# Kernel tuning notes

Measured on AMD Instinct MI355X. Metric: run time of the kernel, lower is better.

The kernel has to match this reference:

```python
import jax, jax.numpy as jnp
import numpy as np

N_EMBED = 256
B, T = 2, 8192


def setup_inputs() -> dict:
    key = jax.random.key(0)
    ks = jax.random.split(key, 7)
    s = 1.0 / np.sqrt(N_EMBED)  # ~nn.Linear init scale
    return {
        "x": jax.random.normal(ks[0], (B, T, N_EMBED), dtype=jnp.float32),
        "Wq": jax.random.normal(ks[1], (N_EMBED, N_EMBED), dtype=jnp.float32) * s,
        "bq": jax.random.normal(ks[2], (N_EMBED,), dtype=jnp.float32) * s,
        "Wk": jax.random.normal(ks[3], (N_EMBED, N_EMBED), dtype=jnp.float32) * s,
        "bk": jax.random.normal(ks[4], (N_EMBED,), dtype=jnp.float32) * s,
        "Wv": jax.random.normal(ks[5], (N_EMBED, N_EMBED), dtype=jnp.float32) * s,
        "bv": jax.random.normal(ks[6], (N_EMBED,), dtype=jnp.float32) * s,
    }


def reference(x, Wq, bq, Wk, bk, Wv, bv):
    # q/k/v projections: [B, T, D]
    q = x @ Wq + bq
    k = x @ Wk + bk
    v = x @ Wv + bv
    # Naive attention: full [B, T, T] score matrix, no scale, no mask.
    scores = jnp.einsum("btd,bsd->bts", q, k)
    attn = jax.nn.softmax(scores, axis=-1)
    return jnp.einsum("bts,bsd->btd", attn, v)
```

## Files before the change

### kernel.cpp

```cpp
#include <hip/hip_runtime.h>
#include <stdint.h>

typedef __attribute__((ext_vector_type(4))) float f32x4;
typedef __attribute__((ext_vector_type(16))) float f32x16;
typedef __attribute__((ext_vector_type(8))) short s16x8;
typedef __attribute__((ext_vector_type(4))) short s16x4;
typedef __attribute__((ext_vector_type(4))) unsigned int u32x4;
typedef __attribute__((ext_vector_type(8))) _Float16 f16x8;
typedef __attribute__((ext_vector_type(4))) _Float16 f16x4;

#define MFMA16(a, b, c) __builtin_amdgcn_mfma_f32_16x16x32_bf16((a), (b), (c), 0, 0, 0)
#define MFMA32H(a, b, c) __builtin_amdgcn_mfma_f32_32x32x16_f16((a), (b), (c), 0, 0, 0)


__device__ __forceinline__ unsigned short f2bf(float f) {
  unsigned int u = __float_as_uint(f);
  u += 0x7FFFu + ((u >> 16) & 1u);
  return (unsigned short)(u >> 16);
}
__device__ __forceinline__ float bf2f(unsigned short h) {
  return __uint_as_float(((unsigned int)h) << 16);
}

__global__ void wtrans_kernel(const float* __restrict__ Wq,
                              const float* __restrict__ Wk,
                              const float* __restrict__ Wv,
                              short* __restrict__ wt) {
  int idx = blockIdx.x * 256 + threadIdx.x;
  int w = idx >> 16;
  int rc = idx & 65535;
  int d = rc >> 8;
  int n = rc & 255;
  const float* Ws = (w == 0) ? Wq : ((w == 1) ? Wk : Wv);
  float v = Ws[rc];
  unsigned short hi = f2bf(v);
  unsigned short lo = f2bf(v - bf2f(hi));
  short* th = wt + w * 131072;
  th[n * 256 + d] = (short)hi;
  th[65536 + n * 256 + d] = (short)lo;
}

__global__ __launch_bounds__(256, 2)
void qkv_kernel(const float* __restrict__ x,
                const float* __restrict__ bq,
                const float* __restrict__ bk,
                const float* __restrict__ bv,
                const short* __restrict__ wt,
                short* __restrict__ Qf, short* __restrict__ Kf,
                short* __restrict__ Vt) {
  __shared__ short X[16896];
  int tid = threadIdx.x;
  int r0 = blockIdx.x * 32;
  int bidx = r0 >> 13;
  int tl0 = r0 & 8191;
#pragma unroll
  for (int i = 0; i < 8; i++) {
    int E = i * 1024 + tid * 4;
    int r = E >> 8, col = E & 255;
    f32x4 v = *(const f32x4*)(x + (size_t)(r0 + r) * 256 + col);
    s16x4 h, lo;
#pragma unroll
    for (int j = 0; j < 4; j++) {
      unsigned short hh = f2bf(v[j]);
      h[j] = (short)hh;
      lo[j] = (short)f2bf(v[j] - bf2f(hh));
    }
    *(s16x4*)&X[r * 264 + col] = h;
    *(s16x4*)&X[8448 + r * 264 + col] = lo;
  }
  __syncthreads();

  int lane = tid & 63, wv = tid >> 6;
  int quad = lane >> 4, lq = lane & 15;

  {
    int strip = wv & 1;
    const short* WhT = wt + ((wv < 2) ? 0 : 131072);
    const short* WlT = WhT + 65536;
    f32x4 acc[16];
#pragma unroll
    for (int nt = 0; nt < 16; nt++) acc[nt] = (f32x4){0.f, 0.f, 0.f, 0.f};
    int arow = (strip * 16 + lq) * 264 + quad * 8;
#pragma unroll
    for (int c = 0; c < 8; c++) {
      s16x8 xh = *(const s16x8*)&X[arow + c * 32];
      s16x8 xl = *(const s16x8*)&X[8448 + arow + c * 32];
#pragma unroll
      for (int nt = 0; nt < 16; nt++) {
        int boff = (nt * 16 + lq) * 256 + c * 32 + quad * 8;
        s16x8 wh = *(const s16x8*)(WhT + boff);
        s16x8 wl = *(const s16x8*)(WlT + boff);
        acc[nt] = MFMA16(xh, wh, acc[nt]);
        acc[nt] = MFMA16(xl, wh, acc[nt]);
        acc[nt] = MFMA16(xh, wl, acc[nt]);
      }
    }
    const float* bias = (wv < 2) ? bq : bk;
    _Float16* Of = (_Float16*)((wv < 2) ? Qf : Kf);
#pragma unroll
    for (int nt = 0; nt < 16; nt++) {
      int col = nt * 16 + lq;
      float bb = bias[col];
#pragma unroll
      for (int r = 0; r < 4; r++) {
        int row = r0 + strip * 16 + quad * 4 + r;
        Of[row * 256 + col] = (_Float16)(acc[nt][r] + bb);
      }
    }
  }
  {
    const short* WhT = wt + 262144;
    const short* WlT = wt + 327680;
    f32x4 acc[4][2];
#pragma unroll
    for (int mt = 0; mt < 4; mt++)
#pragma unroll
      for (int nt = 0; nt < 2; nt++) acc[mt][nt] = (f32x4){0.f, 0.f, 0.f, 0.f};
#pragma unroll
    for (int c = 0; c < 8; c++) {
      int co = c * 32 + quad * 8;
      s16x8 xh0 = *(const s16x8*)&X[lq * 264 + co];
      s16x8 xl0 = *(const s16x8*)&X[8448 + lq * 264 + co];
      s16x8 xh1 = *(const s16x8*)&X[(16 + lq) * 264 + co];
      s16x8 xl1 = *(const s16x8*)&X[8448 + (16 + lq) * 264 + co];
#pragma unroll
      for (int mt = 0; mt < 4; mt++) {
        int aoff = (wv * 64 + mt * 16 + lq) * 256 + co;
        s16x8 wh = *(const s16x8*)(WhT + aoff);
        s16x8 wl = *(const s16x8*)(WlT + aoff);
        acc[mt][0] = MFMA16(wh, xh0, acc[mt][0]);
        acc[mt][0] = MFMA16(wl, xh0, acc[mt][0]);
        acc[mt][0] = MFMA16(wh, xl0, acc[mt][0]);
        acc[mt][1] = MFMA16(wh, xh1, acc[mt][1]);
        acc[mt][1] = MFMA16(wl, xh1, acc[mt][1]);
        acc[mt][1] = MFMA16(wh, xl1, acc[mt][1]);
      }
    }
#pragma unroll
    for (int mt = 0; mt < 4; mt++) {
#pragma unroll
      for (int r = 0; r < 4; r++) {
        int drow = wv * 64 + mt * 16 + quad * 4 + r;
        float bb = bv[drow];
#pragma unroll
        for (int nt = 0; nt < 2; nt++) {
          ((_Float16*)Vt)[(bidx * 256 + drow) * 8192 + tl0 + nt * 16 + lq] =
              (_Float16)(acc[mt][nt][r] + bb);
        }
      }
    }
  }
}

__global__ __launch_bounds__(512, 2)
void attn_kernel(const short* __restrict__ Qf, const short* __restrict__ Kf,
                 const short* __restrict__ Vt,
                 float* __restrict__ out, float* __restrict__ O1,
                 float* __restrict__ Mlg) {
  __shared__ short sm[45568];
  short* KL  = sm;
  short* VtL = sm + 16896;
  short* PLb = sm + 35328;
  int tid = threadIdx.x;
  int lane = tid & 63, wv = tid >> 6;
  int lq32 = lane & 31, hh = lane >> 5, h8 = hh * 8;
  int strip = wv & 3, sh = wv >> 2;
  short* PL = PLb + wv * 1280;
  int blk = blockIdx.x;
  int qt = blk >> 1, sblk = blk & 1;
  int row0g = qt * 128;
  int b = row0g >> 13;
  int sbase = b * 8192 + sblk * 4096;

  f16x8 qf[16];
  {
    const _Float16* qrow =
        (const _Float16*)Qf + (size_t)(row0g + strip * 32 + lq32) * 256 + h8;
#pragma unroll
    for (int st = 0; st < 16; st++) qf[st] = *(const f16x8*)(qrow + st * 16);
  }
  float m_ = -__builtin_inff();
  float l_ = 0.f;
  f32x16 Oacc[8];
#pragma unroll
  for (int dt = 0; dt < 8; dt++)
#pragma unroll
    for (int i = 0; i < 16; i++) Oacc[dt][i] = 0.f;

  u32x4 k_r[4], vt_r[4];
#pragma unroll
  for (int i = 0; i < 4; i++) {
    int L = i * 512 + tid;
    int s = L >> 5, g = L & 31;
    int d = L >> 3, g2 = L & 7;
    k_r[i] = *(const u32x4*)(Kf + (size_t)(sbase + s) * 256 + g * 8);
    vt_r[i] = *(const u32x4*)(Vt + (size_t)(b * 256 + d) * 8192 +
                              sblk * 4096 + g2 * 8);
  }

  for (int it = 0; it < 64; it++) {
#pragma unroll
    for (int i = 0; i < 4; i++) {
      int L = i * 512 + tid;
      int s = L >> 5, g = L & 31;
      int d = L >> 3, g2 = L & 7;
      *(u32x4*)&KL[s * 264 + g * 8] = k_r[i];
      *(u32x4*)&VtL[d * 72 + g2 * 8] = vt_r[i];
    }
    __syncthreads();
    {
      int s0n = ((it + 1) & 63) * 64;
#pragma unroll
      for (int i = 0; i < 4; i++) {
        int L = i * 512 + tid;
        int s = L >> 5, g = L & 31;
        int d = L >> 3, g2 = L & 7;
        k_r[i] = *(const u32x4*)(Kf + (size_t)(sbase + s0n + s) * 256 + g * 8);
        vt_r[i] = *(const u32x4*)(Vt + (size_t)(b * 256 + d) * 8192 +
                                  sblk * 4096 + s0n + g2 * 8);
      }
    }
    f32x16 sacc;
#pragma unroll
    for (int i = 0; i < 16; i++) sacc[i] = 0.f;
    int krow = (sh * 32 + lq32) * 264 + h8;
#pragma unroll
    for (int st = 0; st < 16; st++) {
      f16x8 kf = *(const f16x8*)&KL[krow + st * 16];
      sacc = MFMA32H(kf, qf[st], sacc);
    }
    float mx = sacc[0];
#pragma unroll
    for (int i = 1; i < 16; i++) mx = fmaxf(mx, sacc[i]);
    mx = fmaxf(mx, __shfl_xor(mx, 32));
    float mn = fmaxf(m_, mx);
    float alpha = __expf(m_ - mn);
    m_ = mn;
    float rs = 0.f;
#pragma unroll
    for (int i = 0; i < 16; i++) {
      sacc[i] = __expf(sacc[i] - mn);
      rs += sacc[i];
    }
    rs += __shfl_xor(rs, 32);
    l_ = l_ * alpha + rs;
#pragma unroll
    for (int g = 0; g < 4; g++) {
      f16x4 pk;
#pragma unroll
      for (int j = 0; j < 4; j++) pk[j] = (_Float16)sacc[g * 4 + j];
      *(f16x4*)&PL[lq32 * 40 + 8 * g + 4 * hh] = pk;
    }
    if (!__all(alpha == 1.f)) {
#pragma unroll
      for (int dt = 0; dt < 8; dt++) Oacc[dt] = Oacc[dt] * alpha;
    }
    f16x8 pf0 = *(const f16x8*)&PL[lq32 * 40 + h8];
    f16x8 pf1 = *(const f16x8*)&PL[lq32 * 40 + 16 + h8];
#pragma unroll
    for (int dt = 0; dt < 8; dt++) {
      int vrow = (dt * 32 + lq32) * 72 + sh * 32;
      f16x8 vf0 = *(const f16x8*)&VtL[vrow + h8];
      f16x8 vf1 = *(const f16x8*)&VtL[vrow + 16 + h8];
      Oacc[dt] = MFMA32H(vf0, pf0, Oacc[dt]);
      Oacc[dt] = MFMA32H(vf1, pf1, Oacc[dt]);
    }
    __syncthreads();
  }

  float* smf = (float*)sm;
  float* Msh = smf + 16896;
  if (lane < 32) {
    Msh[(sh * 4 + strip) * 32 + lq32] = m_;
    Msh[256 + (sh * 4 + strip) * 32 + lq32] = l_;
  }
  __syncthreads();
  float m1 = Msh[((1 - sh) * 4 + strip) * 32 + lq32];
  float l1 = Msh[256 + ((1 - sh) * 4 + strip) * 32 + lq32];
  float mm = fmaxf(m_, m1);
  float e0 = __expf(m_ - mm);
  float e1 = __expf(m1 - mm);
  float* Opart = (sblk == 0) ? out : O1;
  if (sh == 0 && lane < 32) {
    float lsum = l_ * e0 + l1 * e1;
    int rowq = row0g + strip * 32 + lq32;
    Mlg[sblk * 32768 + rowq * 2] = mm;
    Mlg[sblk * 32768 + rowq * 2 + 1] = lsum;
  }
  float* Ob = smf + strip * 4224;
#pragma unroll
  for (int hd = 0; hd < 2; hd++) {
    __syncthreads();
    if (sh == 1) {
#pragma unroll
      for (int dt2 = 0; dt2 < 4; dt2++) {
        int dt = hd * 4 + dt2;
#pragma unroll
        for (int g = 0; g < 4; g++) {
          f32x4 v = {Oacc[dt][g * 4], Oacc[dt][g * 4 + 1],
                     Oacc[dt][g * 4 + 2], Oacc[dt][g * 4 + 3]};
          *(f32x4*)&Ob[lq32 * 132 + dt2 * 32 + 8 * g + 4 * hh] = v;
        }
      }
    }
    __syncthreads();
    if (sh == 0) {
#pragma unroll
      for (int dt2 = 0; dt2 < 4; dt2++) {
        int dt = hd * 4 + dt2;
#pragma unroll
        for (int g = 0; g < 4; g++) {
          float* ad = &Ob[lq32 * 132 + dt2 * 32 + 8 * g + 4 * hh];
          f32x4 o1 = *(f32x4*)ad;
          f32x4 cmb;
#pragma unroll
          for (int j = 0; j < 4; j++)
            cmb[j] = Oacc[dt][g * 4 + j] * e0 + o1[j] * e1;
          *(f32x4*)ad = cmb;
        }
      }
    }
    __syncthreads();
#pragma unroll
    for (int i = 0; i < 8; i++) {
      int idx = i * 512 + tid;
      int q = idx >> 5, gb = idx & 31;
      f32x4 v = *(f32x4*)&smf[(q >> 5) * 4224 + (q & 31) * 132 + gb * 4];
      *(f32x4*)&Opart[(size_t)(row0g + q) * 256 + hd * 128 + gb * 4] = v;
    }
  }
}

__global__ void merge_kernel(const float* __restrict__ O1,
                             const float* __restrict__ Mlg,
                             float* __restrict__ out) {
  int idx = blockIdx.x * 256 + threadIdx.x;
  int q = idx >> 6, dg = idx & 63;
  float m0 = Mlg[q * 2], l0 = Mlg[q * 2 + 1];
  float m1 = Mlg[32768 + q * 2], l1 = Mlg[32768 + q * 2 + 1];
  float mm = fmaxf(m0, m1);
  float e0 = __expf(m0 - mm), e1 = __expf(m1 - mm);
  float inv = 1.f / (l0 * e0 + l1 * e1);
  f32x4 a = *(const f32x4*)(out + (size_t)q * 256 + dg * 4);
  f32x4 bb = *(const f32x4*)(O1 + (size_t)q * 256 + dg * 4);
  f32x4 r;
#pragma unroll
  for (int j = 0; j < 4; j++) r[j] = (a[j] * e0 + bb[j] * e1) * inv;
  *(f32x4*)(out + (size_t)q * 256 + dg * 4) = r;
}

extern "C" void kernel_launch(void* const* d_in, const int* in_sizes, int n_in,
                              void* d_out, int out_size, void* d_ws, size_t ws_size,
                              hipStream_t stream) {
  const float* x  = (const float*)d_in[0];
  const float* Wq = (const float*)d_in[1];
  const float* bq = (const float*)d_in[2];
  const float* Wk = (const float*)d_in[3];
  const float* bk = (const float*)d_in[4];
  const float* Wv = (const float*)d_in[5];
  const float* bv = (const float*)d_in[6];
  float* out = (float*)d_out;
  short* ws = (short*)d_ws;
  short* wt = ws;
  short* Qf = ws + 393216;
  short* Kf = Qf + 4194304;
  short* Vt = Kf + 4194304;
  float* O1  = (float*)(ws + 12976128);
  float* Mlg = (float*)ws;
  hipLaunchKernelGGL(wtrans_kernel, dim3(768), dim3(256), 0, stream, Wq, Wk, Wv, wt);
  hipLaunchKernelGGL(qkv_kernel, dim3(512), dim3(256), 0, stream,
                     x, bq, bk, bv, wt, Qf, Kf, Vt);
  hipLaunchKernelGGL(attn_kernel, dim3(256), dim3(512), 0, stream,
                     Qf, Kf, Vt, out, O1, Mlg);
  hipLaunchKernelGGL(merge_kernel, dim3(4096), dim3(256), 0, stream,
                     O1, Mlg, out);
}
```

Before: 385.8 us.

## Double-buffer K/V tiles in LDS and pass P via lane shuffles

K and V tiles are now double-buffered in shared memory, so the next tile is written after compute and only one barrier per iteration is needed. The softmax probabilities are packed to fp16 and exchanged across half-waves with shuffles instead of going through a per-wave LDS scratch area. This cuts barrier stalls and LDS traffic, but enlarges shared memory, which likely reduces resident blocks per CU.

After: 410.4 us. +6.4%, slower.

```diff
diff --git a/kernel.cpp b/kernel.cpp
--- a/kernel.cpp
+++ b/kernel.cpp
@@ -7,7 +7,7 @@
 typedef __attribute__((ext_vector_type(4))) short s16x4;
 typedef __attribute__((ext_vector_type(4))) unsigned int u32x4;
 typedef __attribute__((ext_vector_type(8))) _Float16 f16x8;
-typedef __attribute__((ext_vector_type(4))) _Float16 f16x4;
+typedef __attribute__((ext_vector_type(2))) _Float16 f16x2;
 
 #define MFMA16(a, b, c) __builtin_amdgcn_mfma_f32_16x16x32_bf16((a), (b), (c), 0, 0, 0)
 #define MFMA32H(a, b, c) __builtin_amdgcn_mfma_f32_32x32x16_f16((a), (b), (c), 0, 0, 0)
@@ -20,6 +20,12 @@
 }
 __device__ __forceinline__ float bf2f(unsigned short h) {
   return __uint_as_float(((unsigned int)h) << 16);
+}
+__device__ __forceinline__ unsigned int packh2(float a, float b) {
+  f16x2 t;
+  t[0] = (_Float16)a;
+  t[1] = (_Float16)b;
+  return *(unsigned int*)&t;
 }
 
 __global__ void wtrans_kernel(const float* __restrict__ Wq,
@@ -157,15 +163,11 @@
                  const short* __restrict__ Vt,
                  float* __restrict__ out, float* __restrict__ O1,
                  float* __restrict__ Mlg) {
-  __shared__ short sm[45568];
-  short* KL  = sm;
-  short* VtL = sm + 16896;
-  short* PLb = sm + 35328;
+  __shared__ short sm[70656];
   int tid = threadIdx.x;
   int lane = tid & 63, wv = tid >> 6;
   int lq32 = lane & 31, hh = lane >> 5, h8 = hh * 8;
   int strip = wv & 3, sh = wv >> 2;
-  short* PL = PLb + wv * 1280;
   int blk = blockIdx.x;
   int qt = blk >> 1, sblk = blk & 1;
   int row0g = qt * 128;
@@ -197,19 +199,20 @@
     vt_r[i] = *(const u32x4*)(Vt + (size_t)(b * 256 + d) * 8192 +
                               sblk * 4096 + g2 * 8);
   }
+#pragma unroll
+  for (int i = 0; i < 4; i++) {
+    int L = i * 512 + tid;
+    int s = L >> 5, g = L & 31;
+    int d = L >> 3, g2 = L & 7;
+    *(u32x4*)&sm[s * 264 + g * 8] = k_r[i];
+    *(u32x4*)&sm[16896 + d * 72 + g2 * 8] = vt_r[i];
+  }
 
   for (int it = 0; it < 64; it++) {
-#pragma unroll
-    for (int i = 0; i < 4; i++) {
-      int L = i * 512 + tid;
-      int s = L >> 5, g = L & 31;
-      int d = L >> 3, g2 = L & 7;
-      *(u32x4*)&KL[s * 264 + g * 8] = k_r[i];
-      *(u32x4*)&VtL[d * 72 + g2 * 8] = vt_r[i];
-    }
+    short* cur = sm + (it & 1) * 35328;
     __syncthreads();
-    {
-      int s0n = ((it + 1) & 63) * 64;
+    if (it < 63) {
+      int s0n = (it + 1) * 64;
 #pragma unroll
       for (int i = 0; i < 4; i++) {
         int L = i * 512 + tid;
@@ -226,7 +229,7 @@
     int krow = (sh * 32 + lq32) * 264 + h8;
 #pragma unroll
     for (int st = 0; st < 16; st++) {
-      f16x8 kf = *(const f16x8*)&KL[krow + st * 16];
+      f16x8 kf = *(const f16x8*)&cur[krow + st * 16];
       sacc = MFMA32H(kf, qf[st], sacc);
     }
     float mx = sacc[0];
@@ -244,28 +247,50 @@
     }
     rs += __shfl_xor(rs, 32);
     l_ = l_ * alpha + rs;
+    unsigned int pkk[8], pxx[8];
 #pragma unroll
     for (int g = 0; g < 4; g++) {
-      f16x4 pk;
-#pragma unroll
-      for (int j = 0; j < 4; j++) pk[j] = (_Float16)sacc[g * 4 + j];
-      *(f16x4*)&PL[lq32 * 40 + 8 * g + 4 * hh] = pk;
-    }
+#pragma unroll
+      for (int jp = 0; jp < 2; jp++)
+        pkk[g * 2 + jp] = packh2(sacc[4 * g + 2 * jp], sacc[4 * g + 2 * jp + 1]);
+    }
+#pragma unroll
+    for (int i = 0; i < 8; i++) pxx[i] = (unsigned int)__shfl_xor((int)pkk[i], 32);
+    u32x4 F0, F1;
+    F0[0] = hh ? pxx[2] : pkk[0];
+    F0[1] = hh ? pxx[3] : pkk[1];
+    F0[2] = hh ? pkk[2] : pxx[0];
+    F0[3] = hh ? pkk[3] : pxx[1];
+    F1[0] = hh ? pxx[6] : pkk[4];
+    F1[1] = hh ? pxx[7] : pkk[5];
+    F1[2] = hh ? pkk[6] : pxx[4];
+    F1[3] = hh ? pkk[7] : pxx[5];
+    f16x8 pf0 = *(f16x8*)&F0;
+    f16x8 pf1 = *(f16x8*)&F1;
     if (!__all(alpha == 1.f)) {
 #pragma unroll
       for (int dt = 0; dt < 8; dt++) Oacc[dt] = Oacc[dt] * alpha;
     }
-    f16x8 pf0 = *(const f16x8*)&PL[lq32 * 40 + h8];
-    f16x8 pf1 = *(const f16x8*)&PL[lq32 * 40 + 16 + h8];
+    const short* vb = cur + 16896;
 #pragma unroll
     for (int dt = 0; dt < 8; dt++) {
       int vrow = (dt * 32 + lq32) * 72 + sh * 32;
-      f16x8 vf0 = *(const f16x8*)&VtL[vrow + h8];
-      f16x8 vf1 = *(const f16x8*)&VtL[vrow + 16 + h8];
+      f16x8 vf0 = *(const f16x8*)&vb[vrow + h8];
+      f16x8 vf1 = *(const f16x8*)&vb[vrow + 16 + h8];
       Oacc[dt] = MFMA32H(vf0, pf0, Oacc[dt]);
       Oacc[dt] = MFMA32H(vf1, pf1, Oacc[dt]);
     }
-    __syncthreads();
+    if (it < 63) {
+      short* nxt = sm + ((it + 1) & 1) * 35328;
+#pragma unroll
+      for (int i = 0; i < 4; i++) {
+        int L = i * 512 + tid;
+        int s = L >> 5, g = L & 31;
+        int d = L >> 3, g2 = L & 7;
+        *(u32x4*)&nxt[s * 264 + g * 8] = k_r[i];
+        *(u32x4*)&nxt[16896 + d * 72 + g2 * 8] = vt_r[i];
+      }
+    }
   }
 
   float* smf = (float*)sm;
```
